# Kernel optimization log

Hardware: AMD Instinct MI355X
Metric: run time of the kernel (lower is better)

Reference implementation:

```python
import jax, jax.numpy as jnp
import numpy as np

N = 45056      # 2048 instances * 22 machines
E = 720896     # avg degree 16
FEA = 60       # max_num*6
HID = 256
MACH = 22
NEG_SLOPE = 0.01


def setup_inputs() -> dict:
    key = jax.random.key(0)
    ks = jax.random.split(key, 20)
    x = jax.random.normal(ks[0], (N, FEA), dtype=jnp.float32)
    edge_index = jax.random.randint(ks[1], (2, E), 0, N, dtype=jnp.int64)
    edge_weight = jax.random.uniform(ks[2], (E,), dtype=jnp.float32)

    def lin(k, fan_in, fan_out):
        s = 1.0 / np.sqrt(fan_in)
        kw, kb = jax.random.split(k)
        W = jax.random.uniform(kw, (fan_in, fan_out), minval=-s, maxval=s, dtype=jnp.float32)
        b = jax.random.uniform(kb, (fan_out,), minval=-s, maxval=s, dtype=jnp.float32)
        return W, b

    W1, b1 = lin(ks[3], FEA, HID)
    W2, b2 = lin(ks[4], HID, HID)
    mlp_in = MACH * (HID + FEA)  # 6952
    Wf0, bf0 = lin(ks[5], mlp_in, HID)
    Wf1, bf1 = lin(ks[6], HID, HID)
    Wf2, bf2 = lin(ks[7], HID, HID)
    Wo, bo = lin(ks[8], HID, 4)
    return {"x": x, "edge_index": edge_index, "edge_weight": edge_weight,
            "W1": W1, "b1": b1, "W2": W2, "b2": b2,
            "Wf0": Wf0, "bf0": bf0, "Wf1": Wf1, "bf1": bf1,
            "Wf2": Wf2, "bf2": bf2, "Wo": Wo, "bo": bo}


def _gcn_conv(h, W, b, row, col, norm, n):
    # h' = scatter_add(norm * (hW)[row] -> col) + b   (PyG GCNConv)
    hw = h @ W                                  # [N, out]
    msg = hw[row] * norm[:, None]               # [E+N, out]
    out = jax.ops.segment_sum(msg, col, num_segments=n)
    return out + b


def reference(x, edge_index, edge_weight, W1, b1, W2, b2,
              Wf0, bf0, Wf1, bf1, Wf2, bf2, Wo, bo):
    n = x.shape[0]
    # gcn_norm with self-loops (fill_value=1.0), symmetric normalization
    loop = jnp.arange(n, dtype=edge_index.dtype)
    row = jnp.concatenate([edge_index[0], loop])
    col = jnp.concatenate([edge_index[1], loop])
    ew = jnp.concatenate([edge_weight, jnp.ones((n,), dtype=edge_weight.dtype)])
    deg = jax.ops.segment_sum(ew, col, num_segments=n)
    dinv = jnp.where(deg > 0, jax.lax.rsqrt(jnp.maximum(deg, 1e-12)), 0.0)
    norm = dinv[row] * ew * dinv[col]

    h = _gcn_conv(x, W1, b1, row, col, norm, n)
    h = jax.nn.leaky_relu(h, NEG_SLOPE)
    # dropout p=0.5 is identity in eval mode
    h = _gcn_conv(h, W2, b2, row, col, norm, n)
    h = jax.nn.leaky_relu(h, NEG_SLOPE)

    h = jnp.concatenate([h, x], axis=1)         # [N, HID+FEA]
    flat = h.reshape(n // MACH, -1)             # [B, 22*(HID+FEA)]

    z = jax.nn.leaky_relu(flat @ Wf0 + bf0, NEG_SLOPE)
    z = jax.nn.leaky_relu(z @ Wf1 + bf1, NEG_SLOPE)
    z = jax.nn.leaky_relu(z @ Wf2 + bf2, NEG_SLOPE)
    return z @ Wo + bo                           # [B, 4]
```

## Files before the change

kernel.cpp:

```cpp
#include <hip/hip_runtime.h>
#include <stdint.h>

#define FEA 60
#define HID 256
#define MACH 22
#define PERM 316
#define PERM2 320
#define FLATP2 (MACH * PERM2)
#define NEG 0.01f
#define BCAP 64
#define S0 16
#define KC0 448

typedef __bf16 bf16x8 __attribute__((ext_vector_type(8)));
typedef float f32x4 __attribute__((ext_vector_type(4)));

__device__ __forceinline__ float bf2f(uint16_t u) {
    return __uint_as_float(((uint32_t)u) << 16);
}
__device__ __forceinline__ uint16_t f2bf(float f) {
    uint32_t x = __float_as_uint(f);
    return (uint16_t)((x + 0x7fffu + ((x >> 16) & 1u)) >> 16);
}

__global__ void k_detect_init(const uint32_t* ew_w, const uint32_t* ei_w, int* flags,
                              int* count, float* z0acc, int n) {
    int i = blockIdx.x * blockDim.x + threadIdx.x;
    if (i < n) count[i] = 0;
    z0acc[i] = 0.f;
    if (blockIdx.x == 0) {
        __shared__ int c15, onz;
        if (threadIdx.x == 0) { c15 = 0; onz = 0; }
        __syncthreads();
        int a = 0, b = 0;
        for (int k = threadIdx.x; k < 1024; k += 256) {
            if (ew_w[k] & 0x8000u) a++;
            if (ei_w[2 * k + 1] != 0u) b++;
        }
        atomicAdd(&c15, a); atomicAdd(&onz, b);
        __syncthreads();
        if (threadIdx.x == 0) {
            flags[0] = (c15 <= 100) ? 1 : 0;
            flags[1] = (onz < 8) ? 1 : 0;
        }
    }
}

struct PrepAll {
    const void* xsrc; uint16_t* x64;
    const void* src8[8]; float* dst8[8]; long prefix[9]; int cnt8;
    const void* wf0; uint16_t* wf0t;
    const void* src3[3]; uint16_t* dst3[3];
    const void* w1; uint16_t* w1t;
    const void* ei; const void* ew; int* count; uint2* adj; int E;
    int n;
};

#define NB_CVT 1024
#define NB_TR  492

__global__ __launch_bounds__(256) void k_prep_all(PrepAll a, const int* flags) {
    int isbf = flags[0];
    int b = blockIdx.x;
    int t = threadIdx.x;
    if (b < NB_CVT) {
        long nx = (long)a.n * 64;
        long total = nx + a.prefix[a.cnt8];
        for (long i = (long)b * 256 + t; i < total; i += (long)NB_CVT * 256) {
            if (i < nx) {
                int col = (int)(i & 63);
                long row = i >> 6;
                uint16_t v = 0;
                if (col < FEA) {
                    long s = row * FEA + col;
                    v = isbf ? ((const uint16_t*)a.xsrc)[s] : f2bf(((const float*)a.xsrc)[s]);
                }
                a.x64[i] = v;
            } else {
                long ii = i - nx;
                int tt = 0;
                while (ii >= a.prefix[tt + 1]) tt++;
                long j = ii - a.prefix[tt];
                a.dst8[tt][j] = isbf ? bf2f(((const uint16_t*)a.src8[tt])[j])
                                     : ((const float*)a.src8[tt])[j];
            }
        }
    } else if (b < NB_CVT + NB_TR) {
        __shared__ uint16_t s[64][65];
        int bb = b - NB_CVT;
        if (bb < 440) {
            int g0 = (bb >> 2) * 64, n0 = (bb & 3) * 64;
#pragma unroll
            for (int i = 0; i < 16; i++) {
                int idx = t + i * 256;
                int gg = idx >> 6, nn = idx & 63;
                int gk = g0 + gg;
                int m = gk / PERM2;
                int k2 = gk - m * PERM2;
                uint16_t v = 0;
                if (k2 < PERM) {
                    long off = (long)(m * PERM + k2) * HID + n0 + nn;
                    v = isbf ? ((const uint16_t*)a.wf0)[off] : f2bf(((const float*)a.wf0)[off]);
                }
                s[gg][nn] = v;
            }
            __syncthreads();
#pragma unroll
            for (int i = 0; i < 16; i++) {
                int idx = t + i * 256;
                int nn = idx >> 6, gg = idx & 63;
                a.wf0t[(long)(n0 + nn) * FLATP2 + g0 + gg] = s[gg][nn];
            }
        } else if (bb < 488) {
            int idx0 = bb - 440;
            int z = idx0 >> 4, r = idx0 & 15;
            int k0 = (r >> 2) * 64, n0 = (r & 3) * 64;
            const void* W = a.src3[z];
            uint16_t* Wt = a.dst3[z];
#pragma unroll
            for (int i = 0; i < 16; i++) {
                int idx = t + i * 256;
                int kk = idx >> 6, nn = idx & 63;
                long off = (long)(k0 + kk) * HID + n0 + nn;
                s[kk][nn] = isbf ? ((const uint16_t*)W)[off] : f2bf(((const float*)W)[off]);
            }
            __syncthreads();
#pragma unroll
            for (int i = 0; i < 16; i++) {
                int idx = t + i * 256;
                int nn = idx >> 6, kk = idx & 63;
                Wt[(long)(n0 + nn) * HID + k0 + kk] = s[kk][nn];
            }
        } else {
            int n0 = (bb - 488) * 64;
#pragma unroll
            for (int i = 0; i < 16; i++) {
                int idx = t + i * 256;
                int kk = idx >> 6, nn = idx & 63;
                uint16_t v = 0;
                if (kk < FEA) {
                    long off = (long)kk * HID + n0 + nn;
                    v = isbf ? ((const uint16_t*)a.w1)[off] : f2bf(((const float*)a.w1)[off]);
                }
                s[kk][nn] = v;
            }
            __syncthreads();
#pragma unroll
            for (int i = 0; i < 16; i++) {
                int idx = t + i * 256;
                int nn = idx >> 6, kk = idx & 63;
                a.w1t[(long)(n0 + nn) * 64 + kk] = s[kk][nn];
            }
        }
    } else {
        int e0 = ((b - NB_CVT - NB_TR) * 256 + t) * 2;
        int E = a.E;
        if (e0 >= E) return;
        int i64 = flags[1];
        int r0, r1 = -1, c0, c1 = -1;
        if (i64) {
            const long long* pr = (const long long*)a.ei + e0;
            const long long* pc = (const long long*)a.ei + E + e0;
            r0 = (int)pr[0]; c0 = (int)pc[0];
            if (e0 + 1 < E) { r1 = (int)pr[1]; c1 = (int)pc[1]; }
        } else {
            const int* pr = (const int*)a.ei + e0;
            const int* pc = (const int*)a.ei + E + e0;
            r0 = pr[0]; c0 = pc[0];
            if (e0 + 1 < E) { r1 = pr[1]; c1 = pc[1]; }
        }
        float w0, w1 = 0.f;
        if (isbf) {
            uint32_t ww = ((const uint32_t*)a.ew)[e0 >> 1];
            w0 = bf2f((uint16_t)(ww & 0xffff));
            w1 = bf2f((uint16_t)(ww >> 16));
        } else {
            float2 f = ((const float2*)a.ew)[e0 >> 1];
            w0 = f.x; w1 = f.y;
        }
        int p0 = atomicAdd(&a.count[c0], 1);
        unsigned long long v0 = (unsigned long long)(uint32_t)r0 |
                                ((unsigned long long)__float_as_uint(w0) << 32);
        __builtin_nontemporal_store(v0, (unsigned long long*)&a.adj[((long)c0 << 6) + p0]);
        if (c1 >= 0) {
            int p1 = atomicAdd(&a.count[c1], 1);
            unsigned long long v1 = (unsigned long long)(uint32_t)r1 |
                                    ((unsigned long long)__float_as_uint(w1) << 32);
            __builtin_nontemporal_store(v1, (unsigned long long*)&a.adj[((long)c1 << 6) + p1]);
        }
    }
}

__global__ void k_rowsum(const int* count, const uint2* adj, float* dinv, int n) {
    int i = blockIdx.x * blockDim.x + threadIdx.x;
    if (i >= n) return;
    int cnt = count[i];
    const uint2* row = adj + ((long)i << 6);
    double d = 1.0;
    for (int p = 0; p < cnt; p++) d += (double)__uint_as_float(row[p].y);
    dinv[i] = (float)(1.0 / sqrt(d));
}

__global__ __launch_bounds__(256) void k_aggx(const uint16_t* __restrict__ x64,
                                              const float* __restrict__ dinv,
                                              const int* __restrict__ count,
                                              const uint2* __restrict__ adj,
                                              uint16_t* __restrict__ xa, int n) {
    __shared__ uint2 sadj[16][16];
    int cg = blockIdx.x & 1;
    int ng = blockIdx.x >> 1;
    int slot = threadIdx.x >> 4;
    int l = threadIdx.x & 15;
    int node = ng * 16 + slot;
    if (node >= n) return;
    const uint32_t* xu = (const uint32_t*)x64;
    int cbase = cg * 16;
    float di = dinv[node];
    float c2 = di * di;
    uint32_t h = xu[(long)node * 32 + cbase + l];
    float a0 = c2 * bf2f((uint16_t)(h & 0xffff));
    float a1 = c2 * bf2f((uint16_t)(h >> 16));
    int cnt = count[node];
    const uint2* row = adj + ((long)node << 6);
    for (int base = 0; base < cnt; base += 16) {
        int m = cnt - base; if (m > 16) m = 16;
        if (l < m) {
            uint2 a = row[base + l];
            float w = __uint_as_float(a.y) * dinv[a.x] * di;
            uint2 p; p.x = a.x; p.y = __float_as_uint(w);
            sadj[slot][l] = p;
        }
        int t = 0;
        for (; t + 4 <= m; t += 4) {
            uint2 e0 = sadj[slot][t], e1 = sadj[slot][t + 1];
            uint2 e2 = sadj[slot][t + 2], e3 = sadj[slot][t + 3];
            uint32_t v0 = xu[(long)e0.x * 32 + cbase + l];
            uint32_t v1 = xu[(long)e1.x * 32 + cbase + l];
            uint32_t v2 = xu[(long)e2.x * 32 + cbase + l];
            uint32_t v3 = xu[(long)e3.x * 32 + cbase + l];
            float w0 = __uint_as_float(e0.y), w1 = __uint_as_float(e1.y);
            float w2 = __uint_as_float(e2.y), w3 = __uint_as_float(e3.y);
            a0 += w0 * bf2f((uint16_t)(v0 & 0xffff)); a1 += w0 * bf2f((uint16_t)(v0 >> 16));
            a0 += w1 * bf2f((uint16_t)(v1 & 0xffff)); a1 += w1 * bf2f((uint16_t)(v1 >> 16));
            a0 += w2 * bf2f((uint16_t)(v2 & 0xffff)); a1 += w2 * bf2f((uint16_t)(v2 >> 16));
            a0 += w3 * bf2f((uint16_t)(v3 & 0xffff)); a1 += w3 * bf2f((uint16_t)(v3 >> 16));
        }
        for (; t < m; t++) {
            uint2 e0 = sadj[slot][t];
            uint32_t v0 = xu[(long)e0.x * 32 + cbase + l];
            float w0 = __uint_as_float(e0.y);
            a0 += w0 * bf2f((uint16_t)(v0 & 0xffff));
            a1 += w0 * bf2f((uint16_t)(v0 >> 16));
        }
    }
    ((uint32_t*)xa)[(long)node * 32 + cbase + l] =
        (uint32_t)f2bf(a0) | ((uint32_t)f2bf(a1) << 16);
}

__global__ __launch_bounds__(256) void k_aggb(const uint16_t* __restrict__ hw,
                                              const float* __restrict__ dinv,
                                              const int* __restrict__ count,
                                              const uint2* __restrict__ adj,
                                              const float* __restrict__ bias,
                                              uint16_t* __restrict__ out, int n) {
    __shared__ uint2 sadj[16][16];
    int cg = blockIdx.x & 7;
    int ng = blockIdx.x >> 3;
    int slot = threadIdx.x >> 4;
    int l = threadIdx.x & 15;
    int node = ng * 16 + slot;
    if (node >= n) return;
    const uint32_t* hwu = (const uint32_t*)hw;
    int cbase = cg * 16;
    float di = dinv[node];
    float c2 = di * di;
    uint32_t h = hwu[(long)node * 128 + cbase + l];
    float a0 = c2 * bf2f((uint16_t)(h & 0xffff));
    float a1 = c2 * bf2f((uint16_t)(h >> 16));
    int cnt = count[node];
    const uint2* row = adj + ((long)node << 6);
    for (int base = 0; base < cnt; base += 16) {
        int m = cnt - base; if (m > 16) m = 16;
        if (l < m) {
            uint2 a = row[base + l];
            float w = __uint_as_float(a.y) * dinv[a.x] * di;
            uint2 p; p.x = a.x; p.y = __float_as_uint(w);
            sadj[slot][l] = p;
        }
        int t = 0;
        for (; t + 4 <= m; t += 4) {
            uint2 e0 = sadj[slot][t], e1 = sadj[slot][t + 1];
            uint2 e2 = sadj[slot][t + 2], e3 = sadj[slot][t + 3];
            uint32_t v0 = hwu[(long)e0.x * 128 + cbase + l];
            uint32_t v1 = hwu[(long)e1.x * 128 + cbase + l];
            uint32_t v2 = hwu[(long)e2.x * 128 + cbase + l];
            uint32_t v3 = hwu[(long)e3.x * 128 + cbase + l];
            float w0 = __uint_as_float(e0.y), w1 = __uint_as_float(e1.y);
            float w2 = __uint_as_float(e2.y), w3 = __uint_as_float(e3.y);
            a0 += w0 * bf2f((uint16_t)(v0 & 0xffff)); a1 += w0 * bf2f((uint16_t)(v0 >> 16));
            a0 += w1 * bf2f((uint16_t)(v1 & 0xffff)); a1 += w1 * bf2f((uint16_t)(v1 >> 16));
            a0 += w2 * bf2f((uint16_t)(v2 & 0xffff)); a1 += w2 * bf2f((uint16_t)(v2 >> 16));
            a0 += w3 * bf2f((uint16_t)(v3 & 0xffff)); a1 += w3 * bf2f((uint16_t)(v3 >> 16));
        }
        for (; t < m; t++) {
            uint2 e0 = sadj[slot][t];
            uint32_t v0 = hwu[(long)e0.x * 128 + cbase + l];
            float w0 = __uint_as_float(e0.y);
            a0 += w0 * bf2f((uint16_t)(v0 & 0xffff));
            a1 += w0 * bf2f((uint16_t)(v0 >> 16));
        }
    }
    float2 bv = ((const float2*)bias)[cbase + l];
    a0 += bv.x; a1 += bv.y;
    a0 = a0 > 0.f ? a0 : NEG * a0;
    a1 = a1 > 0.f ? a1 : NEG * a1;
    ((uint32_t*)out)[(long)node * 128 + cbase + l] =
        (uint32_t)f2bf(a0) | ((uint32_t)f2bf(a1) << 16);
}

__global__ __launch_bounds__(256) void k_mgemm(const uint16_t* __restrict__ A,
                                               const uint16_t* __restrict__ Bt,
                                               uint16_t* __restrict__ outb,
                                               const float* __restrict__ bias,
                                               int M, int K, int act) {
    __shared__ uint16_t As[128 * 40];
    __shared__ uint16_t Bs[128 * 40];
    int tid = threadIdx.x;
    int lane = tid & 63, wv = tid >> 6;
    int quad = lane >> 4, l15 = lane & 15;
    int row0 = blockIdx.y * 128, col0 = blockIdx.x * 128;
    int arow = (wv >> 1) * 64;
    int bcol = (wv & 1) * 64;

    f32x4 acc[4][4];
#pragma unroll
    for (int i = 0; i < 4; i++)
#pragma unroll
        for (int j = 0; j < 4; j++) acc[i][j] = (f32x4){0.f, 0.f, 0.f, 0.f};

    for (int kc = 0; kc < K; kc += 32) {
#pragma unroll
        for (int i = 0; i < 2; i++) {
            int idx = tid + i * 256;
            int r = idx >> 2, cq = idx & 3;
            uint4 va = *(const uint4*)(A + (long)(row0 + r) * K + kc + cq * 8);
            *(uint4*)(&As[r * 40 + cq * 8]) = va;
            uint4 vb = *(const uint4*)(Bt + (long)(col0 + r) * K + kc + cq * 8);
            *(uint4*)(&Bs[r * 40 + cq * 8]) = vb;
        }
        __syncthreads();
        bf16x8 af[4], bfr[4];
#pragma unroll
        for (int i = 0; i < 4; i++)
            af[i] = __builtin_bit_cast(bf16x8,
                *(const uint4*)(&As[(arow + i * 16 + l15) * 40 + quad * 8]));
#pragma unroll
        for (int j = 0; j < 4; j++)
            bfr[j] = __builtin_bit_cast(bf16x8,
                *(const uint4*)(&Bs[(bcol + j * 16 + l15) * 40 + quad * 8]));
#pragma unroll
        for (int i = 0; i < 4; i++)
#pragma unroll
            for (int j = 0; j < 4; j++)
                acc[i][j] = __builtin_amdgcn_mfma_f32_16x16x32_bf16(af[i], bfr[j], acc[i][j], 0, 0, 0);
        __syncthreads();
    }

#pragma unroll
    for (int i = 0; i < 4; i++)
#pragma unroll
        for (int j = 0; j < 4; j++) {
            int row = row0 + arow + i * 16 + quad * 4;
            int col = col0 + bcol + j * 16 + l15;
#pragma unroll
            for (int reg = 0; reg < 4; reg++) {
                float v = acc[i][j][reg];
                if (bias) v += bias[col];
                if (act) v = v > 0.f ? v : NEG * v;
                outb[(long)(row + reg) * HID + col] = f2bf(v);
            }
        }
}

__global__ __launch_bounds__(256) void k_mgemm_flat(const uint16_t* __restrict__ h2,
                                                    const uint16_t* __restrict__ x64,
                                                    const uint16_t* __restrict__ Bt,
                                                    float* __restrict__ z0acc,
                                                    int M) {
    __shared__ uint16_t As[128 * 40];
    __shared__ uint16_t Bs[128 * 40];
    int tid = threadIdx.x;
    int lane = tid & 63, wv = tid >> 6;
    int quad = lane >> 4, l15 = lane & 15;
    int row0 = blockIdx.y * 128, col0 = blockIdx.x * 128;
    int kbeg = blockIdx.z * KC0;
    int kend = kbeg + KC0; if (kend > FLATP2) kend = FLATP2;
    int arow = (wv >> 1) * 64;
    int bcol = (wv & 1) * 64;

    f32x4 acc[4][4];
#pragma unroll
    for (int i = 0; i < 4; i++)
#pragma unroll
        for (int j = 0; j < 4; j++) acc[i][j] = (f32x4){0.f, 0.f, 0.f, 0.f};

    for (int kc = kbeg; kc < kend; kc += 32) {
#pragma unroll
        for (int i = 0; i < 2; i++) {
            int idx = tid + i * 256;
            int r = idx >> 2, cq = idx & 3;
            int gk = kc + cq * 8;
            int m = gk / PERM2;
            int k2 = gk - m * PERM2;
            long node = (long)(row0 + r) * MACH + m;
            uint4 va = (k2 < HID)
                ? *(const uint4*)(h2 + node * HID + k2)
                : *(const uint4*)(x64 + node * 64 + (k2 - HID));
            *(uint4*)(&As[r * 40 + cq * 8]) = va;
            uint4 vb = *(const uint4*)(Bt + (long)(col0 + r) * FLATP2 + gk);
            *(uint4*)(&Bs[r * 40 + cq * 8]) = vb;
        }
        __syncthreads();
        bf16x8 af[4], bfr[4];
#pragma unroll
        for (int i = 0; i < 4; i++)
            af[i] = __builtin_bit_cast(bf16x8,
                *(const uint4*)(&As[(arow + i * 16 + l15) * 40 + quad * 8]));
#pragma unroll
        for (int j = 0; j < 4; j++)
            bfr[j] = __builtin_bit_cast(bf16x8,
                *(const uint4*)(&Bs[(bcol + j * 16 + l15) * 40 + quad * 8]));
#pragma unroll
        for (int i = 0; i < 4; i++)
#pragma unroll
            for (int j = 0; j < 4; j++)
                acc[i][j] = __builtin_amdgcn_mfma_f32_16x16x32_bf16(af[i], bfr[j], acc[i][j], 0, 0, 0);
        __syncthreads();
    }

#pragma unroll
    for (int i = 0; i < 4; i++)
#pragma unroll
        for (int j = 0; j < 4; j++) {
            int row = row0 + arow + i * 16 + quad * 4;
            int col = col0 + bcol + j * 16 + l15;
#pragma unroll
            for (int reg = 0; reg < 4; reg++)
                atomicAdd(&z0acc[(long)(row + reg) * HID + col], acc[i][j][reg]);
        }
}

__global__ __launch_bounds__(256) void k_tail(const float* __restrict__ z0acc,
                                              const float* __restrict__ bf0,
                                              const uint16_t* __restrict__ Wf1t,
                                              const float* __restrict__ bf1,
                                              const uint16_t* __restrict__ Wf2t,
                                              const float* __restrict__ bf2,
                                              const float* __restrict__ Wo,
                                              const float* __restrict__ bo,
                                              void* out, const int* flags) {
    __shared__ uint16_t z0s[16 * 256];
    __shared__ uint16_t z1s[16 * 256];
    __shared__ uint16_t z2s[16 * 256];
    int tid = threadIdx.x;
    int lane = tid & 63, wv = tid >> 6;
    int quad = lane >> 4, l15 = lane & 15;
    int rows0 = blockIdx.x * 16;
    int nw = wv * 64;

    for (int i = tid; i < 16 * 256; i += 256) {
        int rr = i >> 8, cc = i & 255;
        float v = z0acc[(long)(rows0 + rr) * HID + cc] + bf0[cc];
        v = v > 0.f ? v : NEG * v;
        z0s[i] = f2bf(v);
    }
    __syncthreads();

    {
        f32x4 acc[4];
#pragma unroll
        for (int j = 0; j < 4; j++) acc[j] = (f32x4){0.f, 0.f, 0.f, 0.f};
        for (int kc = 0; kc < HID; kc += 32) {
            bf16x8 a = __builtin_bit_cast(bf16x8,
                *(const uint4*)(&z0s[l15 * 256 + kc + quad * 8]));
#pragma unroll
            for (int j = 0; j < 4; j++) {
                bf16x8 b = __builtin_bit_cast(bf16x8,
                    *(const uint4*)(Wf1t + (long)(nw + j * 16 + l15) * HID + kc + quad * 8));
                acc[j] = __builtin_amdgcn_mfma_f32_16x16x32_bf16(a, b, acc[j], 0, 0, 0);
            }
        }
#pragma unroll
        for (int j = 0; j < 4; j++) {
            int col = nw + j * 16 + l15;
            float bj = bf1[col];
#pragma unroll
            for (int reg = 0; reg < 4; reg++) {
                float v = acc[j][reg] + bj;
                v = v > 0.f ? v : NEG * v;
                z1s[(quad * 4 + reg) * 256 + col] = f2bf(v);
            }
        }
    }
    __syncthreads();

    {
        f32x4 acc[4];
#pragma unroll
        for (int j = 0; j < 4; j++) acc[j] = (f32x4){0.f, 0.f, 0.f, 0.f};
        for (int kc = 0; kc < HID; kc += 32) {
            bf16x8 a = __builtin_bit_cast(bf16x8,
                *(const uint4*)(&z1s[l15 * 256 + kc + quad * 8]));
#pragma unroll
            for (int j = 0; j < 4; j++) {
                bf16x8 b = __builtin_bit_cast(bf16x8,
                    *(const uint4*)(Wf2t + (long)(nw + j * 16 + l15) * HID + kc + quad * 8));
                acc[j] = __builtin_amdgcn_mfma_f32_16x16x32_bf16(a, b, acc[j], 0, 0, 0);
            }
        }
#pragma unroll
        for (int j = 0; j < 4; j++) {
            int col = nw + j * 16 + l15;
            float bj = bf2[col];
#pragma unroll
            for (int reg = 0; reg < 4; reg++) {
                float v = acc[j][reg] + bj;
                v = v > 0.f ? v : NEG * v;
                z2s[(quad * 4 + reg) * 256 + col] = f2bf(v);
            }
        }
    }
    __syncthreads();

    if (tid < 64) {
        int r = tid >> 2, o = tid & 3;
        float acc = bo[o];
        for (int k = 0; k < HID; k++)
            acc += bf2f(z2s[r * 256 + k]) * Wo[k * 4 + o];
        long idx = (long)(rows0 + r) * 4 + o;
        if (flags[0]) ((uint16_t*)out)[idx] = f2bf(acc);
        else          ((float*)out)[idx] = acc;
    }
}

extern "C" void kernel_launch(void* const* d_in, const int* in_sizes, int n_in,
                              void* d_out, int out_size, void* d_ws, size_t ws_size,
                              hipStream_t stream) {
    const int N  = in_sizes[0] / FEA;
    const int E  = in_sizes[2];
    const int Bn = N / MACH;

    char* ws = (char*)d_ws;
    size_t off = 0;
    auto alloc = [&](size_t bytes) -> char* {
        char* p = ws + off;
        off = (off + bytes + 255) & ~(size_t)255;
        return p;
    };

    int*      flags  = (int*)     alloc(64);
    uint16_t* x64    = (uint16_t*)alloc((size_t)N * 64 * 2);
    uint16_t* xa     = (uint16_t*)alloc((size_t)N * 64 * 2);
    uint16_t* W1t    = (uint16_t*)alloc((size_t)HID * 64 * 2);
    uint16_t* W2t    = (uint16_t*)alloc((size_t)HID * HID * 2);
    uint16_t* Wf0t   = (uint16_t*)alloc((size_t)HID * FLATP2 * 2);
    uint16_t* Wf1t   = (uint16_t*)alloc((size_t)HID * HID * 2);
    uint16_t* Wf2t   = (uint16_t*)alloc((size_t)HID * HID * 2);
    float*    b1     = (float*)   alloc(HID * 4);
    float*    b2     = (float*)   alloc(HID * 4);
    float*    bf0    = (float*)   alloc(HID * 4);
    float*    bf1    = (float*)   alloc(HID * 4);
    float*    bf2    = (float*)   alloc(HID * 4);
    float*    Wo     = (float*)   alloc((size_t)HID * 4 * 4);
    float*    bo     = (float*)   alloc(4 * 4);
    int*      count  = (int*)     alloc((size_t)N * 4);
    uint2*    adj    = (uint2*)   alloc((size_t)N * BCAP * 8);
    float*    dinv   = (float*)   alloc((size_t)N * 4);
    uint16_t* P      = (uint16_t*)alloc((size_t)N * HID * 2);
    uint16_t* Q      = (uint16_t*)alloc((size_t)N * HID * 2);
    float*    z0acc  = (float*)   alloc((size_t)Bn * HID * 4);
    (void)ws_size; (void)n_in; (void)out_size;

    k_detect_init<<<(Bn * HID) / 256, 256, 0, stream>>>(
        (const uint32_t*)d_in[2], (const uint32_t*)d_in[1], flags, count, z0acc, N);

    PrepAll pa{};
    pa.xsrc = d_in[0]; pa.x64 = x64;
    const void* s8[7] = { d_in[4], d_in[6], d_in[8], d_in[10], d_in[12], d_in[13], d_in[14] };
    float* d8[7] = { b1, b2, bf0, bf1, bf2, Wo, bo };
    long n8[7] = { HID, HID, HID, HID, HID, (long)HID * 4, 4 };
    pa.cnt8 = 7;
    pa.prefix[0] = 0;
    for (int t = 0; t < 7; t++) { pa.src8[t] = s8[t]; pa.dst8[t] = d8[t]; pa.prefix[t + 1] = pa.prefix[t] + n8[t]; }
    pa.prefix[8] = pa.prefix[7];
    pa.wf0 = d_in[7]; pa.wf0t = Wf0t;
    pa.src3[0] = d_in[5];  pa.dst3[0] = W2t;
    pa.src3[1] = d_in[9];  pa.dst3[1] = Wf1t;
    pa.src3[2] = d_in[11]; pa.dst3[2] = Wf2t;
    pa.w1 = d_in[3]; pa.w1t = W1t;
    pa.ei = d_in[1]; pa.ew = d_in[2]; pa.count = count; pa.adj = adj; pa.E = E;
    pa.n = N;
    int nb_sc = (E / 2 + 255) / 256;
    k_prep_all<<<NB_CVT + NB_TR + nb_sc, 256, 0, stream>>>(pa, flags);

    k_rowsum<<<(N + 255) / 256, 256, 0, stream>>>(count, adj, dinv, N);

    k_aggx<<<2 * ((N + 15) / 16), 256, 0, stream>>>(x64, dinv, count, adj, xa, N);
    k_mgemm<<<dim3(2, N / 128), 256, 0, stream>>>(xa, W1t, P, b1, N, 64, 1);

    k_mgemm<<<dim3(2, N / 128), 256, 0, stream>>>(P, W2t, Q, nullptr, N, HID, 0);
    k_aggb<<<8 * ((N + 15) / 16), 256, 0, stream>>>(Q, dinv, count, adj, b2, P, N);

    k_mgemm_flat<<<dim3(2, Bn / 128, S0), 256, 0, stream>>>(P, x64, Wf0t, z0acc, Bn);

    k_tail<<<Bn / 16, 256, 0, stream>>>(z0acc, bf0, Wf1t, bf1, Wf2t, bf2, Wo, bo,
                                        d_out, flags);
}
```

Before: 370.5 us.

## Block feature layouts per column group and schedule gathers with XCC-affine work queues

Node features for x and the second GCN hidden layer are now stored column-block-major, 32 bf16 per block, so each gather kernel touches one contiguous slab. The aggregation kernels become persistent blocks that pull node tiles from atomic work queues, starting on a column group chosen by the XCC id. The aim is to keep each slab resident in that die's L2 and cut cache-miss traffic on the random neighbour gathers. Adjacency reads use nontemporal loads, and the final output dot product is split across all threads with a shared-memory reduction. The cost is atomic contention on the queue counters and extra indexing in the GEMM epilogue and in the loads of the flat GEMM.

```diff
diff --git a/kernel.cpp b/kernel.cpp
--- a/kernel.cpp
+++ b/kernel.cpp
@@ -22,11 +22,22 @@
     uint32_t x = __float_as_uint(f);
     return (uint16_t)((x + 0x7fffu + ((x >> 16) & 1u)) >> 16);
 }
+__device__ __forceinline__ uint2 nt_load_u2(const uint2* p) {
+    unsigned long long raw = __builtin_nontemporal_load((const unsigned long long*)p);
+    uint2 v; v.x = (uint32_t)raw; v.y = (uint32_t)(raw >> 32);
+    return v;
+}
+__device__ __forceinline__ int xcc_id() {
+    int x;
+    asm volatile("s_getreg_b32 %0, hwreg(HW_REG_XCC_ID)" : "=s"(x));
+    return x & 7;
+}
 
 __global__ void k_detect_init(const uint32_t* ew_w, const uint32_t* ei_w, int* flags,
-                              int* count, float* z0acc, int n) {
+                              int* count, float* z0acc, int* wq, int n) {
     int i = blockIdx.x * blockDim.x + threadIdx.x;
     if (i < n) count[i] = 0;
+    if (i < 16) wq[i] = 0;
     z0acc[i] = 0.f;
     if (blockIdx.x == 0) {
         __shared__ int c15, onz;
@@ -47,7 +58,7 @@
 }
 
 struct PrepAll {
-    const void* xsrc; uint16_t* x64;
+    const void* xsrc; uint16_t* x64b;
     const void* src8[8]; float* dst8[8]; long prefix[9]; int cnt8;
     const void* wf0; uint16_t* wf0t;
     const void* src3[3]; uint16_t* dst3[3];
@@ -75,7 +86,7 @@
                     long s = row * FEA + col;
                     v = isbf ? ((const uint16_t*)a.xsrc)[s] : f2bf(((const float*)a.xsrc)[s]);
                 }
-                a.x64[i] = v;
+                a.x64b[((long)(col >> 5) * a.n + row) * 32 + (col & 31)] = v;
             } else {
                 long ii = i - nx;
                 int tt = 0;
@@ -197,132 +208,163 @@
     int cnt = count[i];
     const uint2* row = adj + ((long)i << 6);
     double d = 1.0;
-    for (int p = 0; p < cnt; p++) d += (double)__uint_as_float(row[p].y);
+    for (int p = 0; p < cnt; p++) {
+        uint2 v = nt_load_u2(&row[p]);
+        d += (double)__uint_as_float(v.y);
+    }
     dinv[i] = (float)(1.0 / sqrt(d));
 }
 
-__global__ __launch_bounds__(256) void k_aggx(const uint16_t* __restrict__ x64,
+__global__ __launch_bounds__(256) void k_aggx(const uint16_t* __restrict__ x64b,
                                               const float* __restrict__ dinv,
                                               const int* __restrict__ count,
                                               const uint2* __restrict__ adj,
-                                              uint16_t* __restrict__ xa, int n) {
+                                              uint16_t* __restrict__ xa,
+                                              int* __restrict__ wq, int n) {
     __shared__ uint2 sadj[16][16];
-    int cg = blockIdx.x & 1;
-    int ng = blockIdx.x >> 1;
+    __shared__ int sT;
     int slot = threadIdx.x >> 4;
     int l = threadIdx.x & 15;
-    int node = ng * 16 + slot;
-    if (node >= n) return;
-    const uint32_t* xu = (const uint32_t*)x64;
-    int cbase = cg * 16;
-    float di = dinv[node];
-    float c2 = di * di;
-    uint32_t h = xu[(long)node * 32 + cbase + l];
-    float a0 = c2 * bf2f((uint16_t)(h & 0xffff));
-    float a1 = c2 * bf2f((uint16_t)(h >> 16));
-    int cnt = count[node];
-    const uint2* row = adj + ((long)node << 6);
-    for (int base = 0; base < cnt; base += 16) {
-        int m = cnt - base; if (m > 16) m = 16;
-        if (l < m) {
-            uint2 a = row[base + l];
-            float w = __uint_as_float(a.y) * dinv[a.x] * di;
-            uint2 p; p.x = a.x; p.y = __float_as_uint(w);
-            sadj[slot][l] = p;
-        }
-        int t = 0;
-        for (; t + 4 <= m; t += 4) {
-            uint2 e0 = sadj[slot][t], e1 = sadj[slot][t + 1];
-            uint2 e2 = sadj[slot][t + 2], e3 = sadj[slot][t + 3];
-            uint32_t v0 = xu[(long)e0.x * 32 + cbase + l];
-            uint32_t v1 = xu[(long)e1.x * 32 + cbase + l];
-            uint32_t v2 = xu[(long)e2.x * 32 + cbase + l];
-            uint32_t v3 = xu[(long)e3.x * 32 + cbase + l];
-            float w0 = __uint_as_float(e0.y), w1 = __uint_as_float(e1.y);
-            float w2 = __uint_as_float(e2.y), w3 = __uint_as_float(e3.y);
-            a0 += w0 * bf2f((uint16_t)(v0 & 0xffff)); a1 += w0 * bf2f((uint16_t)(v0 >> 16));
-            a0 += w1 * bf2f((uint16_t)(v1 & 0xffff)); a1 += w1 * bf2f((uint16_t)(v1 >> 16));
-            a0 += w2 * bf2f((uint16_t)(v2 & 0xffff)); a1 += w2 * bf2f((uint16_t)(v2 >> 16));
-            a0 += w3 * bf2f((uint16_t)(v3 & 0xffff)); a1 += w3 * bf2f((uint16_t)(v3 >> 16));
-        }
-        for (; t < m; t++) {
-            uint2 e0 = sadj[slot][t];
-            uint32_t v0 = xu[(long)e0.x * 32 + cbase + l];
-            float w0 = __uint_as_float(e0.y);
-            a0 += w0 * bf2f((uint16_t)(v0 & 0xffff));
-            a1 += w0 * bf2f((uint16_t)(v0 >> 16));
-        }
-    }
-    ((uint32_t*)xa)[(long)node * 32 + cbase + l] =
-        (uint32_t)f2bf(a0) | ((uint32_t)f2bf(a1) << 16);
-}
-
-__global__ __launch_bounds__(256) void k_aggb(const uint16_t* __restrict__ hw,
+    int T = n >> 4;
+    int cg0 = xcc_id() & 1;
+    const uint32_t* xu = (const uint32_t*)x64b;
+    for (int go = 0; go < 2; go++) {
+        int g = (cg0 + go) & 1;
+        long gbase = (long)g * n;
+        for (;;) {
+            __syncthreads();
+            if (threadIdx.x == 0) sT = atomicAdd(&wq[8 + g], 2);
+            __syncthreads();
+            int t0 = sT;
+            if (t0 >= T) break;
+            int tmax = (t0 + 2 < T) ? t0 + 2 : T;
+            for (int tt = t0; tt < tmax; tt++) {
+                int node = tt * 16 + slot;
+                float di = dinv[node];
+                float c2 = di * di;
+                uint32_t h = xu[(gbase + node) * 16 + l];
+                float a0 = c2 * bf2f((uint16_t)(h & 0xffff));
+                float a1 = c2 * bf2f((uint16_t)(h >> 16));
+                int cnt = count[node];
+                const uint2* row = adj + ((long)node << 6);
+                for (int base = 0; base < cnt; base += 16) {
+                    int m = cnt - base; if (m > 16) m = 16;
+                    if (l < m) {
+                        uint2 a = nt_load_u2(&row[base + l]);
+                        float w = __uint_as_float(a.y) * dinv[a.x] * di;
+                        uint2 p; p.x = a.x; p.y = __float_as_uint(w);
+                        sadj[slot][l] = p;
+                    }
+                    int t2 = 0;
+                    for (; t2 + 4 <= m; t2 += 4) {
+                        uint2 e0 = sadj[slot][t2],     e1 = sadj[slot][t2 + 1];
+                        uint2 e2 = sadj[slot][t2 + 2], e3 = sadj[slot][t2 + 3];
+                        uint32_t v0 = xu[(gbase + e0.x) * 16 + l];
+                        uint32_t v1 = xu[(gbase + e1.x) * 16 + l];
+                        uint32_t v2 = xu[(gbase + e2.x) * 16 + l];
+                        uint32_t v3 = xu[(gbase + e3.x) * 16 + l];
+                        float w0 = __uint_as_float(e0.y), w1 = __uint_as_float(e1.y);
+                        float w2 = __uint_as_float(e2.y), w3 = __uint_as_float(e3.y);
+                        a0 += w0 * bf2f((uint16_t)(v0 & 0xffff)); a1 += w0 * bf2f((uint16_t)(v0 >> 16));
+                        a0 += w1 * bf2f((uint16_t)(v1 & 0xffff)); a1 += w1 * bf2f((uint16_t)(v1 >> 16));
+                        a0 += w2 * bf2f((uint16_t)(v2 & 0xffff)); a1 += w2 * bf2f((uint16_t)(v2 >> 16));
+                        a0 += w3 * bf2f((uint16_t)(v3 & 0xffff)); a1 += w3 * bf2f((uint16_t)(v3 >> 16));
+                    }
+                    for (; t2 < m; t2++) {
+                        uint2 e0 = sadj[slot][t2];
+                        uint32_t v0 = xu[(gbase + e0.x) * 16 + l];
+                        float w0 = __uint_as_float(e0.y);
+                        a0 += w0 * bf2f((uint16_t)(v0 & 0xffff));
+                        a1 += w0 * bf2f((uint16_t)(v0 >> 16));
+                    }
+                }
+                ((uint32_t*)xa)[(long)node * 32 + g * 16 + l] =
+                    (uint32_t)f2bf(a0) | ((uint32_t)f2bf(a1) << 16);
+            }
+        }
+    }
+}
+
+__global__ __launch_bounds__(256) void k_aggb(const uint16_t* __restrict__ hwb,
                                               const float* __restrict__ dinv,
                                               const int* __restrict__ count,
                                               const uint2* __restrict__ adj,
                                               const float* __restrict__ bias,
-                                              uint16_t* __restrict__ out, int n) {
+                                              uint16_t* __restrict__ out,
+                                              int* __restrict__ wq, int n) {
     __shared__ uint2 sadj[16][16];
-    int cg = blockIdx.x & 7;
-    int ng = blockIdx.x >> 3;
+    __shared__ int sT;
     int slot = threadIdx.x >> 4;
     int l = threadIdx.x & 15;
-    int node = ng * 16 + slot;
-    if (node >= n) return;
-    const uint32_t* hwu = (const uint32_t*)hw;
-    int cbase = cg * 16;
-    float di = dinv[node];
-    float c2 = di * di;
-    uint32_t h = hwu[(long)node * 128 + cbase + l];
-    float a0 = c2 * bf2f((uint16_t)(h & 0xffff));
-    float a1 = c2 * bf2f((uint16_t)(h >> 16));
-    int cnt = count[node];
-    const uint2* row = adj + ((long)node << 6);
-    for (int base = 0; base < cnt; base += 16) {
-        int m = cnt - base; if (m > 16) m = 16;
-        if (l < m) {
-            uint2 a = row[base + l];
-            float w = __uint_as_float(a.y) * dinv[a.x] * di;
-            uint2 p; p.x = a.x; p.y = __float_as_uint(w);
-            sadj[slot][l] = p;
-        }
-        int t = 0;
-        for (; t + 4 <= m; t += 4) {
-            uint2 e0 = sadj[slot][t], e1 = sadj[slot][t + 1];
-            uint2 e2 = sadj[slot][t + 2], e3 = sadj[slot][t + 3];
-            uint32_t v0 = hwu[(long)e0.x * 128 + cbase + l];
-            uint32_t v1 = hwu[(long)e1.x * 128 + cbase + l];
-            uint32_t v2 = hwu[(long)e2.x * 128 + cbase + l];
-            uint32_t v3 = hwu[(long)e3.x * 128 + cbase + l];
-            float w0 = __uint_as_float(e0.y), w1 = __uint_as_float(e1.y);
-            float w2 = __uint_as_float(e2.y), w3 = __uint_as_float(e3.y);
-            a0 += w0 * bf2f((uint16_t)(v0 & 0xffff)); a1 += w0 * bf2f((uint16_t)(v0 >> 16));
-            a0 += w1 * bf2f((uint16_t)(v1 & 0xffff)); a1 += w1 * bf2f((uint16_t)(v1 >> 16));
-            a0 += w2 * bf2f((uint16_t)(v2 & 0xffff)); a1 += w2 * bf2f((uint16_t)(v2 >> 16));
-            a0 += w3 * bf2f((uint16_t)(v3 & 0xffff)); a1 += w3 * bf2f((uint16_t)(v3 >> 16));
-        }
-        for (; t < m; t++) {
-            uint2 e0 = sadj[slot][t];
-            uint32_t v0 = hwu[(long)e0.x * 128 + cbase + l];
-            float w0 = __uint_as_float(e0.y);
-            a0 += w0 * bf2f((uint16_t)(v0 & 0xffff));
-            a1 += w0 * bf2f((uint16_t)(v0 >> 16));
-        }
-    }
-    float2 bv = ((const float2*)bias)[cbase + l];
-    a0 += bv.x; a1 += bv.y;
-    a0 = a0 > 0.f ? a0 : NEG * a0;
-    a1 = a1 > 0.f ? a1 : NEG * a1;
-    ((uint32_t*)out)[(long)node * 128 + cbase + l] =
-        (uint32_t)f2bf(a0) | ((uint32_t)f2bf(a1) << 16);
+    int T = n >> 4;
+    int cg0 = xcc_id() & 7;
+    const uint32_t* hwu = (const uint32_t*)hwb;
+    for (int go = 0; go < 8; go++) {
+        int g = (cg0 + go) & 7;
+        long gbase = (long)g * n;
+        float2 bv = ((const float2*)bias)[g * 16 + l];
+        for (;;) {
+            __syncthreads();
+            if (threadIdx.x == 0) sT = atomicAdd(&wq[g], 2);
+            __syncthreads();
+            int t0 = sT;
+            if (t0 >= T) break;
+            int tmax = (t0 + 2 < T) ? t0 + 2 : T;
+            for (int tt = t0; tt < tmax; tt++) {
+                int node = tt * 16 + slot;
+                float di = dinv[node];
+                float c2 = di * di;
+                uint32_t h = hwu[(gbase + node) * 16 + l];
+                float a0 = c2 * bf2f((uint16_t)(h & 0xffff));
+                float a1 = c2 * bf2f((uint16_t)(h >> 16));
+                int cnt = count[node];
+                const uint2* row = adj + ((long)node << 6);
+                for (int base = 0; base < cnt; base += 16) {
+                    int m = cnt - base; if (m > 16) m = 16;
+                    if (l < m) {
+                        uint2 a = nt_load_u2(&row[base + l]);
+                        float w = __uint_as_float(a.y) * dinv[a.x] * di;
+                        uint2 p; p.x = a.x; p.y = __float_as_uint(w);
+                        sadj[slot][l] = p;
+                    }
+                    int t2 = 0;
+                    for (; t2 + 4 <= m; t2 += 4) {
+                        uint2 e0 = sadj[slot][t2],     e1 = sadj[slot][t2 + 1];
+                        uint2 e2 = sadj[slot][t2 + 2], e3 = sadj[slot][t2 + 3];
+                        uint32_t v0 = hwu[(gbase + e0.x) * 16 + l];
+                        uint32_t v1 = hwu[(gbase + e1.x) * 16 + l];
+                        uint32_t v2 = hwu[(gbase + e2.x) * 16 + l];
+                        uint32_t v3 = hwu[(gbase + e3.x) * 16 + l];
+                        float w0 = __uint_as_float(e0.y), w1 = __uint_as_float(e1.y);
+                        float w2 = __uint_as_float(e2.y), w3 = __uint_as_float(e3.y);
+                        a0 += w0 * bf2f((uint16_t)(v0 & 0xffff)); a1 += w0 * bf2f((uint16_t)(v0 >> 16));
+                        a0 += w1 * bf2f((uint16_t)(v1 & 0xffff)); a1 += w1 * bf2f((uint16_t)(v1 >> 16));
+                        a0 += w2 * bf2f((uint16_t)(v2 & 0xffff)); a1 += w2 * bf2f((uint16_t)(v2 >> 16));
+                        a0 += w3 * bf2f((uint16_t)(v3 & 0xffff)); a1 += w3 * bf2f((uint16_t)(v3 >> 16));
+                    }
+                    for (; t2 < m; t2++) {
+                        uint2 e0 = sadj[slot][t2];
+                        uint32_t v0 = hwu[(gbase + e0.x) * 16 + l];
+                        float w0 = __uint_as_float(e0.y);
+                        a0 += w0 * bf2f((uint16_t)(v0 & 0xffff));
+                        a1 += w0 * bf2f((uint16_t)(v0 >> 16));
+                    }
+                }
+                a0 += bv.x; a1 += bv.y;
+                a0 = a0 > 0.f ? a0 : NEG * a0;
+                a1 = a1 > 0.f ? a1 : NEG * a1;
+                ((uint32_t*)out)[(long)node * 128 + g * 16 + l] =
+                    (uint32_t)f2bf(a0) | ((uint32_t)f2bf(a1) << 16);
+            }
+        }
+    }
 }
 
 __global__ __launch_bounds__(256) void k_mgemm(const uint16_t* __restrict__ A,
                                                const uint16_t* __restrict__ Bt,
                                                uint16_t* __restrict__ outb,
                                                const float* __restrict__ bias,
-                                               int M, int K, int act) {
+                                               int M, int K, int act, int blkout) {
     __shared__ uint16_t As[128 * 40];
     __shared__ uint16_t Bs[128 * 40];
     int tid = threadIdx.x;
@@ -377,16 +419,19 @@
                 float v = acc[i][j][reg];
                 if (bias) v += bias[col];
                 if (act) v = v > 0.f ? v : NEG * v;
-                outb[(long)(row + reg) * HID + col] = f2bf(v);
+                long o = blkout
+                    ? ((long)(col >> 5) * M + (row + reg)) * 32 + (col & 31)
+                    : (long)(row + reg) * HID + col;
+                outb[o] = f2bf(v);
             }
         }
 }
 
 __global__ __launch_bounds__(256) void k_mgemm_flat(const uint16_t* __restrict__ h2,
-                                                    const uint16_t* __restrict__ x64,
+                                                    const uint16_t* __restrict__ x64b,
                                                     const uint16_t* __restrict__ Bt,
                                                     float* __restrict__ z0acc,
-                                                    int M) {
+                                                    int M, int Ntot) {
     __shared__ uint16_t As[128 * 40];
     __shared__ uint16_t Bs[128 * 40];
     int tid = threadIdx.x;
@@ -413,9 +458,13 @@
             int m = gk / PERM2;
             int k2 = gk - m * PERM2;
             long node = (long)(row0 + r) * MACH + m;
-            uint4 va = (k2 < HID)
-                ? *(const uint4*)(h2 + node * HID + k2)
-                : *(const uint4*)(x64 + node * 64 + (k2 - HID));
+            uint4 va;
+            if (k2 < HID) {
+                va = *(const uint4*)(h2 + node * HID + k2);
+            } else {
+                int c = k2 - HID;
+                va = *(const uint4*)(x64b + ((long)(c >> 5) * Ntot + node) * 32 + (c & 31));
+            }
             *(uint4*)(&As[r * 40 + cq * 8]) = va;
             uint4 vb = *(const uint4*)(Bt + (long)(col0 + r) * FLATP2 + gk);
             *(uint4*)(&Bs[r * 40 + cq * 8]) = vb;
@@ -462,6 +511,7 @@
     __shared__ uint16_t z0s[16 * 256];
     __shared__ uint16_t z1s[16 * 256];
     __shared__ uint16_t z2s[16 * 256];
+    __shared__ float hred[256];
     int tid = threadIdx.x;
     int lane = tid & 63, wv = tid >> 6;
     int quad = lane >> 4, l15 = lane & 15;
@@ -532,14 +582,21 @@
     }
     __syncthreads();
 
-    if (tid < 64) {
-        int r = tid >> 2, o = tid & 3;
-        float acc = bo[o];
-        for (int k = 0; k < HID; k++)
+    {
+        int r = tid >> 4, o = (tid >> 2) & 3, part = tid & 3;
+        float acc = 0.f;
+        int k0 = part * 64;
+        for (int k = k0; k < k0 + 64; k++)
             acc += bf2f(z2s[r * 256 + k]) * Wo[k * 4 + o];
+        hred[tid] = acc;
+    }
+    __syncthreads();
+    if ((tid & 3) == 0) {
+        int r = tid >> 4, o = (tid >> 2) & 3;
+        float v = hred[tid] + hred[tid + 1] + hred[tid + 2] + hred[tid + 3] + bo[o];
         long idx = (long)(rows0 + r) * 4 + o;
-        if (flags[0]) ((uint16_t*)out)[idx] = f2bf(acc);
-        else          ((float*)out)[idx] = acc;
+        if (flags[0]) ((uint16_t*)out)[idx] = f2bf(v);
+        else          ((float*)out)[idx] = v;
     }
 }
 
@@ -559,7 +616,8 @@
     };
 
     int*      flags  = (int*)     alloc(64);
-    uint16_t* x64    = (uint16_t*)alloc((size_t)N * 64 * 2);
+    int*      wq     = (int*)     alloc(64);
+    uint16_t* x64b   = (uint16_t*)alloc((size_t)N * 64 * 2);
     uint16_t* xa     = (uint16_t*)alloc((size_t)N * 64 * 2);
     uint16_t* W1t    = (uint16_t*)alloc((size_t)HID * 64 * 2);
     uint16_t* W2t    = (uint16_t*)alloc((size_t)HID * HID * 2);
@@ -582,10 +640,10 @@
     (void)ws_size; (void)n_in; (void)out_size;
 
     k_detect_init<<<(Bn * HID) / 256, 256, 0, stream>>>(
-        (const uint32_t*)d_in[2], (const uint32_t*)d_in[1], flags, count, z0acc, N);
+        (const uint32_t*)d_in[2], (const uint32_t*)d_in[1], flags, count, z0acc, wq, N);
 
     PrepAll pa{};
-    pa.xsrc = d_in[0]; pa.x64 = x64;
+    pa.xsrc = d_in[0]; pa.x64b = x64b;
     const void* s8[7] = { d_in[4], d_in[6], d_in[8], d_in[10], d_in[12], d_in[13], d_in[14] };
     float* d8[7] = { b1, b2, bf0, bf1, bf2, Wo, bo };
     long n8[7] = { HID, HID, HID, HID, HID, (long)HID * 4, 4 };
@@ -605,13 +663,13 @@
 
     k_rowsum<<<(N + 255) / 256, 256, 0, stream>>>(count, adj, dinv, N);
 
-    k_aggx<<<2 * ((N + 15) / 16), 256, 0, stream>>>(x64, dinv, count, adj, xa, N);
-    k_mgemm<<<dim3(2, N / 128), 256, 0, stream>>>(xa, W1t, P, b1, N, 64, 1);
-
-    k_mgemm<<<dim3(2, N / 128), 256, 0, stream>>>(P, W2t, Q, nullptr, N, HID, 0);
-    k_aggb<<<8 * ((N + 15) / 16), 256, 0, stream>>>(Q, dinv, count, adj, b2, P, N);
-
-    k_mgemm_flat<<<dim3(2, Bn / 128, S0), 256, 0, stream>>>(P, x64, Wf0t, z0acc, Bn);
+    k_aggx<<<1024, 256, 0, stream>>>(x64b, dinv, count, adj, xa, wq, N);
+    k_mgemm<<<dim3(2, N / 128), 256, 0, stream>>>(xa, W1t, P, b1, N, 64, 1, 0);
+
+    k_mgemm<<<dim3(2, N / 128), 256, 0, stream>>>(P, W2t, Q, nullptr, N, HID, 0, 1);
+    k_aggb<<<2048, 256, 0, stream>>>(Q, dinv, count, adj, b2, P, wq, N);
+
+    k_mgemm_flat<<<dim3(2, Bn / 128, S0), 256, 0, stream>>>(P, x64b, Wf0t, z0acc, Bn, N);
 
     k_tail<<<Bn / 16, 256, 0, stream>>>(z0acc, bf0, Wf1t, bf1, Wf2t, bf2, Wo, bo,
                                         d_out, flags);
```

Result: slower. 659.3 us (+78.0%).
